# Optimization experiments

Measured on AMD Instinct MI355X. Metric: run time of the kernel, lower is better.

Reference implementation:

```python
import jax, jax.numpy as jnp
import numpy as np

B, S, D, H = 2, 1024, 768, 12
HD = D // H          # head_dim = 64
DFF = 4 * D          # 3072
EPS = 1e-5


def _ln(x, g, b):
    m = x.mean(-1, keepdims=True)
    v = ((x - m) ** 2).mean(-1, keepdims=True)
    return (x - m) * jax.lax.rsqrt(v + EPS) * g + b


def setup_inputs() -> dict:
    key = jax.random.key(0)
    ks = jax.random.split(key, 8)
    w = lambda k, shape: jax.random.normal(k, shape, jnp.float32) * 0.02
    return {
        "inp": jax.random.normal(ks[0], (B, S, D), jnp.float32),
        "attention_mask": jnp.zeros((B, S), bool),  # True = masked out (filled with -inf)
        "rel_matrix": jax.random.randint(ks[1], (B, S, S), -1, 2, jnp.int32),  # values in {-1,0,1}
        "qkv_w": w(ks[2], (3 * D, D)),
        "rel_A": w(ks[3], (3, HD)),        # relative_position_emb_A.weight
        "o_w": w(ks[4], (D, D)),
        "w1": w(ks[5], (DFF, D)), "b1": jnp.zeros((DFF,), jnp.float32),
        "w2": w(ks[6], (D, DFF)), "b2": jnp.zeros((D,), jnp.float32),
        "ln1_g": jnp.ones((D,), jnp.float32), "ln1_b": jnp.zeros((D,), jnp.float32),
        "ln2_g": jnp.ones((D,), jnp.float32), "ln2_b": jnp.zeros((D,), jnp.float32),
    }


def reference(inp, attention_mask, rel_matrix, qkv_w, rel_A, o_w,
              w1, b1, w2, b2, ln1_g, ln1_b, ln2_g, ln2_b):
    x = _ln(inp, ln1_g, ln1_b)
    qkv = x @ qkv_w.T                                  # (B,S,3D)
    q, k, v = jnp.split(qkv, 3, axis=-1)
    heads = lambda t: t.reshape(B, S, H, HD).transpose(0, 2, 1, 3)  # (B,H,S,HD)
    q, k, v = heads(q), heads(k), heads(v)

    # q @ (k + rel_emb)^T without materializing k_aug:
    # q.k^T term plus per-(q,key) relative term gathered from q @ A^T.
    logits = jnp.einsum("bhqd,bhkd->bhqk", q, k)       # (B,H,S,S)
    r = jnp.einsum("bhqd,cd->bhqc", q, rel_A)          # (B,H,S,3)
    idx = (rel_matrix + 1).astype(jnp.int32)           # (B,S,S) in {0,1,2}
    rel = jnp.take_along_axis(r, jnp.broadcast_to(idx[:, None], (B, H, S, S)), axis=-1)
    logits = (logits + rel) / np.sqrt(HD).astype(np.float32)
    # masked_fill: -inf where mask is True
    logits = jnp.where(attention_mask[:, None, None, :], -jnp.inf, logits)

    attn = jax.nn.softmax(logits, axis=-1)
    out = jnp.einsum("bhqk,bhkd->bhqd", attn, v)
    out = out.transpose(0, 2, 1, 3).reshape(B, S, D)
    inp = inp + out @ o_w.T                            # residual (dropout=0)

    h = _ln(inp, ln2_g, ln2_b)
    mlp = jax.nn.relu(h @ w1.T + b1) @ w2.T + b2
    return inp + mlp
```

## Files before the change

### kernel.cpp

```cpp
#include <hip/hip_runtime.h>
#include <hip/hip_bf16.h>

#define BB 2
#define SS 1024
#define DD 768
#define HH 12
#define HD 64
#define DFF 3072
#define EPS 1e-5f
#define BS2 (BB * SS)
#define BSD ((size_t)BS2 * DD)

typedef unsigned short ushort_t;
typedef unsigned char uchar_t;
using short8 = __attribute__((ext_vector_type(8))) short;
using f32x4  = __attribute__((ext_vector_type(4))) float;

__device__ __forceinline__ ushort_t f2bf_rne(float f) {
    union { float f; unsigned u; } x; x.f = f;
    unsigned r = x.u + 0x7fff + ((x.u >> 16) & 1);
    return (ushort_t)(r >> 16);
}
__device__ __forceinline__ float bf2f(short u) {
    union { unsigned i; float f; } x;
    x.i = ((unsigned)(ushort_t)u) << 16;
    return x.f;
}

__global__ __launch_bounds__(256) void cvt_bf16(
    const float* __restrict__ in, ushort_t* __restrict__ out, int n4)
{
    int i = blockIdx.x * 256 + threadIdx.x;
    if (i < n4) {
        float4 v = ((const float4*)in)[i];
        ushort4 o;
        o.x = f2bf_rne(v.x); o.y = f2bf_rne(v.y);
        o.z = f2bf_rne(v.z); o.w = f2bf_rne(v.w);
        ((ushort4*)out)[i] = o;
    }
}

__global__ __launch_bounds__(256) void build_codes(
    const int* __restrict__ rel, const uchar_t* __restrict__ mask,
    unsigned* __restrict__ codes)
{
    int tid = blockIdx.x * 256 + threadIdx.x;
    int l15 = tid & 15;
    int kt  = (tid >> 4) & 15;
    int q   = (tid >> 8) & (SS - 1);
    int b   = tid >> 18;
    const int* rrow = rel + ((size_t)(b * SS + q)) * SS + kt * 64 + l15;
    const uchar_t* mrow = mask + (size_t)b * SS + kt * 64 + l15;
    unsigned o = 0;
#pragma unroll
    for (int nt = 0; nt < 4; ++nt) {
        unsigned c = mrow[nt * 16] ? 3u : (unsigned)(rrow[nt * 16] + 1);
        o |= c << (8 * nt);
    }
    codes[((size_t)(b * SS + q) * 16 + kt) * 16 + l15] = o;
}

__global__ __launch_bounds__(256) void ln_kernel_bf(
    const float* __restrict__ x, const float* __restrict__ g,
    const float* __restrict__ b, ushort_t* __restrict__ y)
{
    const int row = blockIdx.x;
    const float* xr = x + (size_t)row * DD;
    float s = 0.f, ss = 0.f;
    for (int i = threadIdx.x; i < DD; i += 256) {
        float v = xr[i];
        s += v; ss += v * v;
    }
    for (int off = 32; off; off >>= 1) {
        s  += __shfl_down(s,  off);
        ss += __shfl_down(ss, off);
    }
    __shared__ float reds[4], redss[4], bc[2];
    int t = threadIdx.x;
    if ((t & 63) == 0) { reds[t >> 6] = s; redss[t >> 6] = ss; }
    __syncthreads();
    if (t == 0) {
        float S1 = reds[0] + reds[1] + reds[2] + reds[3];
        float S2 = redss[0] + redss[1] + redss[2] + redss[3];
        float mean = S1 / DD;
        float var = S2 / DD - mean * mean;
        bc[0] = mean;
        bc[1] = rsqrtf(var + EPS);
    }
    __syncthreads();
    float mean = bc[0], inv = bc[1];
    ushort_t* yr = y + (size_t)row * DD;
    for (int i = threadIdx.x; i < DD; i += 256) {
        yr[i] = f2bf_rne((xr[i] - mean) * inv * g[i] + b[i]);
    }
}

__global__ __launch_bounds__(256) void init_out_kernel(
    const float* __restrict__ resid, const float* __restrict__ b2,
    float* __restrict__ out, int n4)
{
    int i = blockIdx.x * 256 + threadIdx.x;
    if (i < n4) {
        int col4 = (i * 4) % DD;
        float4 r = ((const float4*)resid)[i];
        float4 b = *(const float4*)(b2 + col4);
        r.x += b.x; r.y += b.y; r.z += b.z; r.w += b.w;
        ((float4*)out)[i] = r;
    }
}

template <bool RELU, bool OUT_BF16, bool HAS_BIAS, bool ATOMIC>
__global__ __launch_bounds__(128) void gemm_wave2(
    const ushort_t* __restrict__ A, const ushort_t* __restrict__ W,
    const float* __restrict__ bias, void* __restrict__ Cout,
    int M, int N, int K, int Ksplit)
{
    __shared__ float red[64 * 64];

    const int n0 = blockIdx.x * 64;
    const int m0 = blockIdx.y * 64;
    const int w  = threadIdx.x >> 6;
    const int l  = threadIdx.x & 63;
    const int l15  = l & 15;
    const int quad = l >> 4;
    const int K2 = Ksplit >> 1;
    const int kb = blockIdx.z * Ksplit + w * K2;

    const ushort_t* aP[4];
    const ushort_t* bP[4];
#pragma unroll
    for (int i = 0; i < 4; ++i) {
        aP[i] = A + (size_t)(m0 + i * 16 + l15) * K + kb + quad * 8;
        bP[i] = W + (size_t)(n0 + i * 16 + l15) * K + kb + quad * 8;
    }

    const int nIter = K2 >> 5;

    f32x4 acc[4][4] = {};
    short8 aF[2][4], bF[2][4];
#pragma unroll
    for (int i = 0; i < 4; ++i) {
        aF[0][i] = *(const short8*)(aP[i]);
        bF[0][i] = *(const short8*)(bP[i]);
    }

    for (int base = 0; base < nIter; base += 2) {
#pragma unroll
        for (int j = 0; j < 2; ++j) {
            const int pre = base + j + 1;
            if (pre < nIter) {
                const int off = pre * 32;
#pragma unroll
                for (int i = 0; i < 4; ++i) {
                    aF[j ^ 1][i] = *(const short8*)(aP[i] + off);
                    bF[j ^ 1][i] = *(const short8*)(bP[i] + off);
                }
            }
#pragma unroll
            for (int i = 0; i < 4; ++i)
#pragma unroll
                for (int jj = 0; jj < 4; ++jj)
                    acc[i][jj] = __builtin_amdgcn_mfma_f32_16x16x32_bf16(
                        aF[j][i], bF[j][jj], acc[i][jj], 0, 0, 0);
        }
    }

    if (w == 1) {
#pragma unroll
        for (int i = 0; i < 4; ++i)
#pragma unroll
            for (int j = 0; j < 4; ++j)
#pragma unroll
                for (int r = 0; r < 4; ++r)
                    red[(((i * 4 + j) * 4) + r) * 64 + l] = acc[i][j][r];
    }
    __syncthreads();
    if (w == 0) {
#pragma unroll
        for (int i = 0; i < 4; ++i)
#pragma unroll
            for (int j = 0; j < 4; ++j)
#pragma unroll
                for (int r = 0; r < 4; ++r)
                    acc[i][j][r] += red[(((i * 4 + j) * 4) + r) * 64 + l];

#pragma unroll
        for (int i = 0; i < 4; ++i) {
            const int row = m0 + i * 16 + quad * 4;
#pragma unroll
            for (int j = 0; j < 4; ++j) {
                const int col = n0 + j * 16 + l15;
                const float bv = HAS_BIAS ? bias[col] : 0.f;
#pragma unroll
                for (int r = 0; r < 4; ++r) {
                    float v = acc[i][j][r] + bv;
                    if (RELU) v = fmaxf(v, 0.f);
                    if (ATOMIC)
                        atomicAdd(&((float*)Cout)[(size_t)(row + r) * N + col], v);
                    else if (OUT_BF16)
                        ((ushort_t*)Cout)[(size_t)(row + r) * N + col] = f2bf_rne(v);
                    else
                        ((float*)Cout)[(size_t)(row + r) * N + col] = v;
                }
            }
        }
    }
}

__global__ __launch_bounds__(256) void attn_mfma_kernel(
    const ushort_t* __restrict__ qkv,
    const unsigned* __restrict__ codes,
    const float* __restrict__ rel_A,
    float* __restrict__ Opart,
    float* __restrict__ lpart)
{
    __shared__ __align__(16) ushort_t Ks[64 * 64];
    __shared__ __align__(16) unsigned Vt2[64 * 36];
    __shared__ __align__(16) ushort_t Ps[64 * 72];
    __shared__ __align__(16) float r3s[64][4];

    const int bx = blockIdx.x;
    const int ks = bx & 1;
    const int qt = (bx >> 1) & 15;
    const int h  = (bx >> 5) % HH;
    const int b  = bx / (32 * HH);
    const int q0 = qt * 64;
    const int t  = threadIdx.x;
    const int w  = t >> 6;
    const int l  = t & 63;
    const int l15  = l & 15;
    const int quad = l >> 4;

    const size_t qrow = (size_t)(b * SS + q0 + w * 16 + l15) * (3 * DD) + h * HD;
    const short8 qf0 = *(const short8*)(qkv + qrow + quad * 8);
    const short8 qf1 = *(const short8*)(qkv + qrow + 32 + quad * 8);

    {
        float rv[3];
#pragma unroll
        for (int c = 0; c < 3; ++c) {
            const float* a = rel_A + c * HD + quad * 8;
            float acc = 0.f;
#pragma unroll
            for (int j = 0; j < 8; ++j) acc += bf2f(qf0[j]) * a[j];
#pragma unroll
            for (int j = 0; j < 8; ++j) acc += bf2f(qf1[j]) * a[32 + j];
            acc += __shfl_xor(acc, 16);
            acc += __shfl_xor(acc, 32);
            rv[c] = acc;
        }
        if (quad == 0) {
            float4 f4 = make_float4(rv[0], rv[1], rv[2], -2.4e31f);
            *(float4*)&r3s[w * 16 + l15][0] = f4;
        }
    }
    __syncthreads();
    float4 r3v[4];
#pragma unroll
    for (int reg = 0; reg < 4; ++reg)
        r3v[reg] = *(const float4*)&r3s[w * 16 + quad * 4 + reg][0];

    float l_run[4] = {0.f, 0.f, 0.f, 0.f};
    f32x4 oacc[4] = {};

    for (int kt = ks * 8; kt < ks * 8 + 8; ++kt) {
        const int k0 = kt * 64;
        __syncthreads();
        {
            const int r  = t >> 3;
            const int cp = t & 7;
            const int cl  = cp ^ (r & 7);
            const ushort_t* g = qkv + (size_t)(b * SS + k0 + r) * (3 * DD) + DD + h * HD + cl * 8;
            __builtin_amdgcn_global_load_lds(
                (const __attribute__((address_space(1))) unsigned*)g,
                (__attribute__((address_space(3))) unsigned*)(Ks + (size_t)t * 8), 16, 0, 0);
            const int r2  = r + 32;
            const int cl2 = cp ^ (r2 & 7);
            const ushort_t* g2 = qkv + (size_t)(b * SS + k0 + r2) * (3 * DD) + DD + h * HD + cl2 * 8;
            __builtin_amdgcn_global_load_lds(
                (const __attribute__((address_space(1))) unsigned*)g2,
                (__attribute__((address_space(3))) unsigned*)(Ks + (size_t)(t + 256) * 8), 16, 0, 0);
        }
        {
            const int kp = t >> 3;
            const int dg = t & 7;
            const ushort_t* g = qkv + (size_t)(b * SS + k0 + 2 * kp) * (3 * DD) + 2 * DD + h * HD + dg * 8;
            short8 va = *(const short8*)g;
            short8 vb = *(const short8*)(g + 3 * DD);
            const int kps = kp ^ ((dg & 7) * 4);
#pragma unroll
            for (int i = 0; i < 8; ++i)
                Vt2[(size_t)(dg * 8 + i) * 36 + kps] =
                    (unsigned)(ushort_t)va[i] | ((unsigned)(ushort_t)vb[i] << 16);
        }
        __syncthreads();

        f32x4 sacc[4] = {};
#pragma unroll
        for (int kc = 0; kc < 2; ++kc) {
            const short8 qv = kc ? qf1 : qf0;
#pragma unroll
            for (int nt = 0; nt < 4; ++nt) {
                const int row = nt * 16 + l15;
                const int cp  = (kc * 4 + quad) ^ (row & 7);
                const short8 kf = *(const short8*)(Ks + (size_t)row * 64 + cp * 8);
                sacc[nt] = __builtin_amdgcn_mfma_f32_16x16x32_bf16(qv, kf, sacc[nt], 0, 0, 0);
            }
        }

#pragma unroll
        for (int reg = 0; reg < 4; ++reg) {
            const int qloc = w * 16 + quad * 4 + reg;
            const unsigned cds = codes[((size_t)(b * SS + q0 + qloc) * 16 + kt) * 16 + l15];
            const float4 r4 = r3v[reg];
#pragma unroll
            for (int nt = 0; nt < 4; ++nt) {
                const unsigned c = (cds >> (8 * nt)) & 0xff;
                float rvv = (c == 0) ? r4.x : (c == 1) ? r4.y : (c == 2) ? r4.z : r4.w;
                const float p = __expf((sacc[nt][reg] + rvv) * 0.125f);
                l_run[reg] += p;
                Ps[(size_t)qloc * 72 + nt * 16 + l15] = f2bf_rne(p);
            }
        }

#pragma unroll
        for (int kc = 0; kc < 2; ++kc) {
            const short8 pf = *(const short8*)(Ps + (size_t)(w * 16 + l15) * 72 + kc * 32 + quad * 8);
#pragma unroll
            for (int dt = 0; dt < 4; ++dt) {
                const int d  = dt * 16 + l15;
                const int dg = d >> 3;
                const int kps0 = (kc * 16 + quad * 4) ^ ((dg & 7) * 4);
                const short8 vf = *(const short8*)((const ushort_t*)&Vt2[(size_t)d * 36 + kps0]);
                oacc[dt] = __builtin_amdgcn_mfma_f32_16x16x32_bf16(pf, vf, oacc[dt], 0, 0, 0);
            }
        }
    }

    float* Op = Opart + (size_t)ks * BSD;
    float* lp = lpart + (size_t)ks * BS2 * HH;
#pragma unroll
    for (int reg = 0; reg < 4; ++reg) {
        float ls = l_run[reg];
        ls += __shfl_xor(ls, 1);
        ls += __shfl_xor(ls, 2);
        ls += __shfl_xor(ls, 4);
        ls += __shfl_xor(ls, 8);
        const int orow = b * SS + q0 + w * 16 + quad * 4 + reg;
#pragma unroll
        for (int dt = 0; dt < 4; ++dt)
            Op[(size_t)orow * DD + h * HD + dt * 16 + l15] = oacc[dt][reg];
        if (l15 == 0) lp[(size_t)orow * HH + h] = ls;
    }
}

__global__ __launch_bounds__(256) void attn_merge(
    const float* __restrict__ Opart, const float* __restrict__ lpart,
    ushort_t* __restrict__ att_bf)
{
    int i = blockIdx.x * 256 + threadIdx.x;
    int row = (i * 4) / DD;
    int h   = ((i * 4) % DD) >> 6;
    float l0 = lpart[(size_t)row * HH + h];
    float l1 = lpart[(size_t)BS2 * HH + (size_t)row * HH + h];
    float inv = 1.0f / (l0 + l1);
    float4 o0 = ((const float4*)Opart)[i];
    float4 o1 = ((const float4*)(Opart + BSD))[i];
    ushort4 o;
    o.x = f2bf_rne((o0.x + o1.x) * inv);
    o.y = f2bf_rne((o0.y + o1.y) * inv);
    o.z = f2bf_rne((o0.z + o1.z) * inv);
    o.w = f2bf_rne((o0.w + o1.w) * inv);
    ((ushort4*)att_bf)[i] = o;
}

extern "C" void kernel_launch(void* const* d_in, const int* in_sizes, int n_in,
                              void* d_out, int out_size, void* d_ws, size_t ws_size,
                              hipStream_t stream) {
    const float* inp   = (const float*)d_in[0];
    const uchar_t* amask = (const uchar_t*)d_in[1];
    const int*   relm  = (const int*)d_in[2];
    const float* qkv_w = (const float*)d_in[3];
    const float* rel_A = (const float*)d_in[4];
    const float* o_w   = (const float*)d_in[5];
    const float* w1    = (const float*)d_in[6];
    const float* b1    = (const float*)d_in[7];
    const float* w2    = (const float*)d_in[8];
    const float* b2    = (const float*)d_in[9];
    const float* ln1_g = (const float*)d_in[10];
    const float* ln1_b = (const float*)d_in[11];
    const float* ln2_g = (const float*)d_in[12];
    const float* ln2_b = (const float*)d_in[13];
    float* out = (float*)d_out;

    char* p = (char*)d_ws;
    ushort_t* x_bf   = (ushort_t*)p; p += BSD * 2;
    ushort_t* att_bf = (ushort_t*)p; p += BSD * 2;
    ushort_t* h_bf   = (ushort_t*)p; p += BSD * 2;
    ushort_t* ff_bf  = (ushort_t*)p; p += (size_t)BS2 * DFF * 2;
    ushort_t* qkvw_bf= (ushort_t*)p; p += (size_t)3 * DD * DD * 2;
    ushort_t* ow_bf  = (ushort_t*)p; p += (size_t)DD * DD * 2;
    ushort_t* w1_bf  = (ushort_t*)p; p += (size_t)DFF * DD * 2;
    ushort_t* w2_bf  = (ushort_t*)p; p += (size_t)DD * DFF * 2;
    ushort_t* qkv_bf = (ushort_t*)p; p += (size_t)BS2 * 3 * DD * 2;
    float*    resid  = (float*)p;    p += BSD * 4;
    float*    Opart  = (float*)p;    p += 2 * BSD * 4;
    float*    lpart  = (float*)p;    p += (size_t)2 * BS2 * HH * 4;
    unsigned* codes  = (unsigned*)p; p += (size_t)BB * SS * SS;

    {
        int n4;
        n4 = 3 * DD * DD / 4;
        cvt_bf16<<<(n4 + 255) / 256, 256, 0, stream>>>(qkv_w, qkvw_bf, n4);
        n4 = DD * DD / 4;
        cvt_bf16<<<(n4 + 255) / 256, 256, 0, stream>>>(o_w, ow_bf, n4);
        n4 = DFF * DD / 4;
        cvt_bf16<<<(n4 + 255) / 256, 256, 0, stream>>>(w1, w1_bf, n4);
        cvt_bf16<<<(n4 + 255) / 256, 256, 0, stream>>>(w2, w2_bf, n4);
        build_codes<<<(BB * SS * 256) / 256, 256, 0, stream>>>(relm, amask, codes);
        hipMemcpyAsync(resid, inp, BSD * 4, hipMemcpyDeviceToDevice, stream);
    }

    ln_kernel_bf<<<BS2, 256, 0, stream>>>(inp, ln1_g, ln1_b, x_bf);

    gemm_wave2<false, true, false, false>
        <<<dim3(3 * DD / 64, BS2 / 64, 1), 128, 0, stream>>>(
        x_bf, qkvw_bf, nullptr, qkv_bf, BS2, 3 * DD, DD, DD);

    attn_mfma_kernel<<<BB * HH * 16 * 2, 256, 0, stream>>>(
        qkv_bf, codes, rel_A, Opart, lpart);
    attn_merge<<<(int)(BSD / 4 / 256), 256, 0, stream>>>(Opart, lpart, att_bf);

    gemm_wave2<false, false, false, true>
        <<<dim3(DD / 64, BS2 / 64, 2), 128, 0, stream>>>(
        att_bf, ow_bf, nullptr, resid, BS2, DD, DD, DD / 2);

    ln_kernel_bf<<<BS2, 256, 0, stream>>>(resid, ln2_g, ln2_b, h_bf);

    gemm_wave2<true, true, true, false>
        <<<dim3(DFF / 64, BS2 / 64, 1), 128, 0, stream>>>(
        h_bf, w1_bf, b1, ff_bf, BS2, DFF, DD, DD);

    init_out_kernel<<<(int)(BSD / 4 + 255) / 256, 256, 0, stream>>>(
        resid, b2, out, (int)(BSD / 4));

    gemm_wave2<false, false, false, true>
        <<<dim3(DD / 64, BS2 / 64, 4), 128, 0, stream>>>(
        ff_bf, w2_bf, nullptr, out, BS2, DD, DFF, DFF / 4);
}
```

Baseline: 294.0 us.

## Replace GEMM with LDS-staged 128x64 tiles, split attention keys 4-way, drop atomics

Replaces the register-direct two-wave GEMM with a 256-thread 128x64 tile kernel. It stages A and B through LDS with global_load_lds, so loaded operands are shared across four waves. Split-K GEMMs now write per-split partials to a pool buffer, and a separate merge kernel adds them to the residual and bias. This replaces float atomics, the memcpy and init_out. Attention splits keys four ways instead of two to get more blocks, at the cost of more partial-output traffic in the merge. The LDS tile loop has no double buffering, so each k-step has two barriers with loads exposed.

```diff
diff --git a/kernel.cpp b/kernel.cpp
--- a/kernel.cpp
+++ b/kernel.cpp
@@ -95,109 +95,113 @@
     }
 }
 
-__global__ __launch_bounds__(256) void init_out_kernel(
-    const float* __restrict__ resid, const float* __restrict__ b2,
-    float* __restrict__ out, int n4)
+template <int Z, bool HAS_BIAS>
+__global__ __launch_bounds__(256) void merge_partials(
+    const float* __restrict__ part, const float* __restrict__ base,
+    const float* __restrict__ bias, float* __restrict__ outp, int n4)
 {
     int i = blockIdx.x * 256 + threadIdx.x;
-    if (i < n4) {
+    if (i >= n4) return;
+    float4 v = ((const float4*)base)[i];
+    if (HAS_BIAS) {
         int col4 = (i * 4) % DD;
-        float4 r = ((const float4*)resid)[i];
-        float4 b = *(const float4*)(b2 + col4);
-        r.x += b.x; r.y += b.y; r.z += b.z; r.w += b.w;
-        ((float4*)out)[i] = r;
-    }
-}
-
-template <bool RELU, bool OUT_BF16, bool HAS_BIAS, bool ATOMIC>
-__global__ __launch_bounds__(128) void gemm_wave2(
+        float4 bv = *(const float4*)(bias + col4);
+        v.x += bv.x; v.y += bv.y; v.z += bv.z; v.w += bv.w;
+    }
+#pragma unroll
+    for (int z = 0; z < Z; ++z) {
+        float4 pz = ((const float4*)(part + (size_t)z * BSD))[i];
+        v.x += pz.x; v.y += pz.y; v.z += pz.z; v.w += pz.w;
+    }
+    ((float4*)outp)[i] = v;
+}
+
+template <bool RELU, bool OUT_BF16, bool HAS_BIAS, bool PARTIAL>
+__global__ __launch_bounds__(256) void gemm_tile(
     const ushort_t* __restrict__ A, const ushort_t* __restrict__ W,
     const float* __restrict__ bias, void* __restrict__ Cout,
     int M, int N, int K, int Ksplit)
 {
-    __shared__ float red[64 * 64];
-
+    __shared__ __align__(16) ushort_t As[512 * 8];
+    __shared__ __align__(16) ushort_t Bs[256 * 8];
+
+    const int t  = threadIdx.x;
     const int n0 = blockIdx.x * 64;
-    const int m0 = blockIdx.y * 64;
-    const int w  = threadIdx.x >> 6;
-    const int l  = threadIdx.x & 63;
+    const int m0 = blockIdx.y * 128;
+    const int kb = blockIdx.z * Ksplit;
+    const int w  = t >> 6;
+    const int l  = t & 63;
+    const int wm = (w & 1) * 64;
+    const int wn = (w >> 1) * 32;
     const int l15  = l & 15;
     const int quad = l >> 4;
-    const int K2 = Ksplit >> 1;
-    const int kb = blockIdx.z * Ksplit + w * K2;
-
-    const ushort_t* aP[4];
-    const ushort_t* bP[4];
-#pragma unroll
-    for (int i = 0; i < 4; ++i) {
-        aP[i] = A + (size_t)(m0 + i * 16 + l15) * K + kb + quad * 8;
-        bP[i] = W + (size_t)(n0 + i * 16 + l15) * K + kb + quad * 8;
-    }
-
-    const int nIter = K2 >> 5;
-
-    f32x4 acc[4][4] = {};
-    short8 aF[2][4], bF[2][4];
-#pragma unroll
-    for (int i = 0; i < 4; ++i) {
-        aF[0][i] = *(const short8*)(aP[i]);
-        bF[0][i] = *(const short8*)(bP[i]);
-    }
-
-    for (int base = 0; base < nIter; base += 2) {
-#pragma unroll
-        for (int j = 0; j < 2; ++j) {
-            const int pre = base + j + 1;
-            if (pre < nIter) {
-                const int off = pre * 32;
-#pragma unroll
-                for (int i = 0; i < 4; ++i) {
-                    aF[j ^ 1][i] = *(const short8*)(aP[i] + off);
-                    bF[j ^ 1][i] = *(const short8*)(bP[i] + off);
-                }
+
+    const ushort_t* gA0 = A + (size_t)(m0 + (t & 127)) * K + kb + (t >> 7) * 8;
+    const ushort_t* gA1 = gA0 + 16;
+    const ushort_t* gB0 = W + (size_t)(n0 + (t & 63)) * K + kb + (t >> 6) * 8;
+    ushort_t* lA0 = &As[(size_t)t * 8];
+    ushort_t* lA1 = &As[(size_t)(t + 256) * 8];
+    ushort_t* lB0 = &Bs[(size_t)t * 8];
+
+    const ushort_t* aptr = &As[(size_t)(quad * 128 + wm + l15) * 8];
+    const ushort_t* bptr = &Bs[(size_t)(quad * 64 + wn + l15) * 8];
+
+    f32x4 acc[4][2] = {};
+
+    for (int k0 = 0; k0 < Ksplit; k0 += 32) {
+        __syncthreads();
+        __builtin_amdgcn_global_load_lds(
+            (const __attribute__((address_space(1))) unsigned int*)(gA0 + k0),
+            (__attribute__((address_space(3))) unsigned int*)lA0, 16, 0, 0);
+        __builtin_amdgcn_global_load_lds(
+            (const __attribute__((address_space(1))) unsigned int*)(gA1 + k0),
+            (__attribute__((address_space(3))) unsigned int*)lA1, 16, 0, 0);
+        __builtin_amdgcn_global_load_lds(
+            (const __attribute__((address_space(1))) unsigned int*)(gB0 + k0),
+            (__attribute__((address_space(3))) unsigned int*)lB0, 16, 0, 0);
+        __syncthreads();
+
+        short8 af[4], bf[2];
+#pragma unroll
+        for (int i = 0; i < 4; ++i)
+            af[i] = *(const short8*)(aptr + (size_t)i * 16 * 8);
+#pragma unroll
+        for (int j = 0; j < 2; ++j)
+            bf[j] = *(const short8*)(bptr + (size_t)j * 16 * 8);
+#pragma unroll
+        for (int i = 0; i < 4; ++i)
+#pragma unroll
+            for (int j = 0; j < 2; ++j)
+                acc[i][j] = __builtin_amdgcn_mfma_f32_16x16x32_bf16(
+                    af[i], bf[j], acc[i][j], 0, 0, 0);
+    }
+
+    if (PARTIAL) {
+        float* Cp = (float*)Cout + (size_t)blockIdx.z * ((size_t)M * N);
+#pragma unroll
+        for (int i = 0; i < 4; ++i) {
+            const int row = m0 + wm + i * 16 + quad * 4;
+#pragma unroll
+            for (int j = 0; j < 2; ++j) {
+                const int col = n0 + wn + j * 16 + l15;
+#pragma unroll
+                for (int r = 0; r < 4; ++r)
+                    Cp[(size_t)(row + r) * N + col] = acc[i][j][r];
             }
-#pragma unroll
-            for (int i = 0; i < 4; ++i)
-#pragma unroll
-                for (int jj = 0; jj < 4; ++jj)
-                    acc[i][jj] = __builtin_amdgcn_mfma_f32_16x16x32_bf16(
-                        aF[j][i], bF[j][jj], acc[i][jj], 0, 0, 0);
-        }
-    }
-
-    if (w == 1) {
-#pragma unroll
-        for (int i = 0; i < 4; ++i)
-#pragma unroll
-            for (int j = 0; j < 4; ++j)
-#pragma unroll
-                for (int r = 0; r < 4; ++r)
-                    red[(((i * 4 + j) * 4) + r) * 64 + l] = acc[i][j][r];
-    }
-    __syncthreads();
-    if (w == 0) {
-#pragma unroll
-        for (int i = 0; i < 4; ++i)
-#pragma unroll
-            for (int j = 0; j < 4; ++j)
-#pragma unroll
-                for (int r = 0; r < 4; ++r)
-                    acc[i][j][r] += red[(((i * 4 + j) * 4) + r) * 64 + l];
-
+        }
+    } else {
 #pragma unroll
         for (int i = 0; i < 4; ++i) {
-            const int row = m0 + i * 16 + quad * 4;
-#pragma unroll
-            for (int j = 0; j < 4; ++j) {
-                const int col = n0 + j * 16 + l15;
+            const int row = m0 + wm + i * 16 + quad * 4;
+#pragma unroll
+            for (int j = 0; j < 2; ++j) {
+                const int col = n0 + wn + j * 16 + l15;
                 const float bv = HAS_BIAS ? bias[col] : 0.f;
 #pragma unroll
                 for (int r = 0; r < 4; ++r) {
                     float v = acc[i][j][r] + bv;
                     if (RELU) v = fmaxf(v, 0.f);
-                    if (ATOMIC)
-                        atomicAdd(&((float*)Cout)[(size_t)(row + r) * N + col], v);
-                    else if (OUT_BF16)
+                    if (OUT_BF16)
                         ((ushort_t*)Cout)[(size_t)(row + r) * N + col] = f2bf_rne(v);
                     else
                         ((float*)Cout)[(size_t)(row + r) * N + col] = v;
@@ -220,10 +224,10 @@
     __shared__ __align__(16) float r3s[64][4];
 
     const int bx = blockIdx.x;
-    const int ks = bx & 1;
-    const int qt = (bx >> 1) & 15;
-    const int h  = (bx >> 5) % HH;
-    const int b  = bx / (32 * HH);
+    const int ks = bx & 3;
+    const int qt = (bx >> 2) & 15;
+    const int h  = (bx >> 6) % HH;
+    const int b  = bx / (64 * HH);
     const int q0 = qt * 64;
     const int t  = threadIdx.x;
     const int w  = t >> 6;
@@ -263,7 +267,7 @@
     float l_run[4] = {0.f, 0.f, 0.f, 0.f};
     f32x4 oacc[4] = {};
 
-    for (int kt = ks * 8; kt < ks * 8 + 8; ++kt) {
+    for (int kt = ks * 4; kt < ks * 4 + 4; ++kt) {
         const int k0 = kt * 64;
         __syncthreads();
         {
@@ -361,16 +365,22 @@
     int i = blockIdx.x * 256 + threadIdx.x;
     int row = (i * 4) / DD;
     int h   = ((i * 4) % DD) >> 6;
-    float l0 = lpart[(size_t)row * HH + h];
-    float l1 = lpart[(size_t)BS2 * HH + (size_t)row * HH + h];
-    float inv = 1.0f / (l0 + l1);
-    float4 o0 = ((const float4*)Opart)[i];
-    float4 o1 = ((const float4*)(Opart + BSD))[i];
+    float lsum = 0.f;
+#pragma unroll
+    for (int z = 0; z < 4; ++z)
+        lsum += lpart[(size_t)z * BS2 * HH + (size_t)row * HH + h];
+    float inv = 1.0f / lsum;
+    float4 os = ((const float4*)Opart)[i];
+#pragma unroll
+    for (int z = 1; z < 4; ++z) {
+        float4 oz = ((const float4*)(Opart + (size_t)z * BSD))[i];
+        os.x += oz.x; os.y += oz.y; os.z += oz.z; os.w += oz.w;
+    }
     ushort4 o;
-    o.x = f2bf_rne((o0.x + o1.x) * inv);
-    o.y = f2bf_rne((o0.y + o1.y) * inv);
-    o.z = f2bf_rne((o0.z + o1.z) * inv);
-    o.w = f2bf_rne((o0.w + o1.w) * inv);
+    o.x = f2bf_rne(os.x * inv);
+    o.y = f2bf_rne(os.y * inv);
+    o.z = f2bf_rne(os.z * inv);
+    o.w = f2bf_rne(os.w * inv);
     ((ushort4*)att_bf)[i] = o;
 }
 
@@ -404,8 +414,8 @@
     ushort_t* w2_bf  = (ushort_t*)p; p += (size_t)DD * DFF * 2;
     ushort_t* qkv_bf = (ushort_t*)p; p += (size_t)BS2 * 3 * DD * 2;
     float*    resid  = (float*)p;    p += BSD * 4;
-    float*    Opart  = (float*)p;    p += 2 * BSD * 4;
-    float*    lpart  = (float*)p;    p += (size_t)2 * BS2 * HH * 4;
+    float*    pool   = (float*)p;    p += 4 * BSD * 4;
+    float*    lpart  = (float*)p;    p += (size_t)4 * BS2 * HH * 4;
     unsigned* codes  = (unsigned*)p; p += (size_t)BB * SS * SS;
 
     {
@@ -418,33 +428,33 @@
         cvt_bf16<<<(n4 + 255) / 256, 256, 0, stream>>>(w1, w1_bf, n4);
         cvt_bf16<<<(n4 + 255) / 256, 256, 0, stream>>>(w2, w2_bf, n4);
         build_codes<<<(BB * SS * 256) / 256, 256, 0, stream>>>(relm, amask, codes);
-        hipMemcpyAsync(resid, inp, BSD * 4, hipMemcpyDeviceToDevice, stream);
     }
 
     ln_kernel_bf<<<BS2, 256, 0, stream>>>(inp, ln1_g, ln1_b, x_bf);
 
-    gemm_wave2<false, true, false, false>
-        <<<dim3(3 * DD / 64, BS2 / 64, 1), 128, 0, stream>>>(
+    gemm_tile<false, true, false, false>
+        <<<dim3(3 * DD / 64, BS2 / 128, 1), 256, 0, stream>>>(
         x_bf, qkvw_bf, nullptr, qkv_bf, BS2, 3 * DD, DD, DD);
 
-    attn_mfma_kernel<<<BB * HH * 16 * 2, 256, 0, stream>>>(
-        qkv_bf, codes, rel_A, Opart, lpart);
-    attn_merge<<<(int)(BSD / 4 / 256), 256, 0, stream>>>(Opart, lpart, att_bf);
-
-    gemm_wave2<false, false, false, true>
-        <<<dim3(DD / 64, BS2 / 64, 2), 128, 0, stream>>>(
-        att_bf, ow_bf, nullptr, resid, BS2, DD, DD, DD / 2);
+    attn_mfma_kernel<<<BB * HH * 16 * 4, 256, 0, stream>>>(
+        qkv_bf, codes, rel_A, pool, lpart);
+    attn_merge<<<(int)(BSD / 4 / 256), 256, 0, stream>>>(pool, lpart, att_bf);
+
+    gemm_tile<false, false, false, true>
+        <<<dim3(DD / 64, BS2 / 128, 2), 256, 0, stream>>>(
+        att_bf, ow_bf, nullptr, pool, BS2, DD, DD, DD / 2);
+    merge_partials<2, false><<<(int)(BSD / 4 / 256), 256, 0, stream>>>(
+        pool, inp, nullptr, resid, (int)(BSD / 4));
 
     ln_kernel_bf<<<BS2, 256, 0, stream>>>(resid, ln2_g, ln2_b, h_bf);
 
-    gemm_wave2<true, true, true, false>
-        <<<dim3(DFF / 64, BS2 / 64, 1), 128, 0, stream>>>(
+    gemm_tile<true, true, true, false>
+        <<<dim3(DFF / 64, BS2 / 128, 1), 256, 0, stream>>>(
         h_bf, w1_bf, b1, ff_bf, BS2, DFF, DD, DD);
 
-    init_out_kernel<<<(int)(BSD / 4 + 255) / 256, 256, 0, stream>>>(
-        resid, b2, out, (int)(BSD / 4));
-
-    gemm_wave2<false, false, false, true>
-        <<<dim3(DD / 64, BS2 / 64, 4), 128, 0, stream>>>(
-        ff_bf, w2_bf, nullptr, out, BS2, DD, DFF, DFF / 4);
-}
+    gemm_tile<false, false, false, true>
+        <<<dim3(DD / 64, BS2 / 128, 4), 256, 0, stream>>>(
+        ff_bf, w2_bf, nullptr, pool, BS2, DD, DFF, DFF / 4);
+    merge_partials<4, true><<<(int)(BSD / 4 / 256), 256, 0, stream>>>(
+        pool, resid, b2, out, (int)(BSD / 4));
+}
```

New measurement: 278.3 us. -5.3%, faster.
